# Kernel tuning notes

Measured on AMD Instinct MI355X. Metric: run time of the kernel, lower is better.

## Reference

```python
import jax, jax.numpy as jnp
import numpy as np

H = 512
B = 32
T = 2048


def setup_inputs() -> dict:
    key = jax.random.key(0)
    ks = jax.random.split(key, 8)
    hidden = jax.random.normal(ks[0], (1, B, H), dtype=jnp.float32)
    encoder_outputs = jax.random.normal(ks[1], (T, B, H), dtype=jnp.float32)
    coverage = jax.random.uniform(ks[2], (B, T), dtype=jnp.float32)
    # nn.Linear(3H, H): weight [H, 3H], bias [H]
    W_attn = jax.random.normal(ks[3], (H, 3 * H), dtype=jnp.float32) / np.sqrt(3 * H)
    b_attn = jax.random.normal(ks[4], (H,), dtype=jnp.float32) / np.sqrt(3 * H)
    # v ~ Normal(0, 1/sqrt(H))
    v = jax.random.normal(ks[5], (H,), dtype=jnp.float32) / np.sqrt(H)
    # nn.Linear(1, H, bias=False): weight [H, 1]
    W_cov = jax.random.normal(ks[6], (H, 1), dtype=jnp.float32)
    return {"hidden": hidden, "encoder_outputs": encoder_outputs, "coverage": coverage,
            "W_attn": W_attn, "b_attn": b_attn, "v": v, "W_cov": W_cov}


def reference(hidden, encoder_outputs, coverage, W_attn, b_attn, v, W_cov):
    # hidden: [1,B,H], encoder_outputs: [T,B,H], coverage: [B,T]
    enc = jnp.transpose(encoder_outputs, (1, 0, 2))          # [B,T,H]
    b, t, h = enc.shape
    hrep = jnp.broadcast_to(hidden[0][:, None, :], (b, t, h))  # [B,T,H]
    # coverage_feature = Linear(1,H,bias=False)(coverage[...,None]) -> outer product
    cov_feat = coverage[..., None] * W_cov[:, 0]               # [B,T,H]
    x = jnp.concatenate([hrep, enc, cov_feat], axis=-1)        # [B,T,3H]
    energy = jax.nn.relu(jnp.einsum('btk,hk->bth', x, W_attn) + b_attn)  # [B,T,H]
    scores = jnp.einsum('bth,h->bt', energy, v)                # [B,T]
    attn_weights = jax.nn.softmax(scores, axis=1)              # softmax over T
    coverage_new = coverage + attn_weights                     # [B,T]
    return attn_weights[:, None, :], coverage_new
```

## Files before the change

### kernel.cpp

```cpp
#include <hip/hip_runtime.h>
#include <hip/hip_bf16.h>

typedef unsigned short u16;
typedef __attribute__((ext_vector_type(8))) short bf16x8;
typedef __attribute__((ext_vector_type(4))) float f32x4;

#define T_DIM 2048
#define B_DIM 32
#define H_DIM 512
#define M_DIM (T_DIM * B_DIM)

__device__ inline unsigned pack2(float a, float b) {
  union { __hip_bfloat162 h2; unsigned u; } c;
  c.h2 = __float22bfloat162_rn(make_float2(a, b));
  return c.u;
}

__global__ __launch_bounds__(256) void prep_kernel(
    const float* __restrict__ hidden, const float* __restrict__ W_attn,
    const float* __restrict__ b_attn, const float* __restrict__ W_cov,
    u16* __restrict__ W2bf, float* __restrict__ r, float* __restrict__ u)
{
  const int tid = blockIdx.x * 256 + threadIdx.x;
  const int pair = tid >> 2;
  const int kq = tid & 3;
  const int b = pair >> 9, h = pair & 511;

  {
    const float* hid = hidden + b * 512 + kq * 128;
    const float* w1 = W_attn + (size_t)h * 1536 + kq * 128;
    float acc = 0.f;
    #pragma unroll 8
    for (int k = 0; k < 128; k += 4) {
      float4 x = *(const float4*)(hid + k);
      float4 w = *(const float4*)(w1 + k);
      acc += x.x * w.x + x.y * w.y + x.z * w.z + x.w * w.w;
    }
    acc += __shfl_xor(acc, 1);
    acc += __shfl_xor(acc, 2);
    if (kq == 0) r[pair] = acc + b_attn[h];
  }

  {
    int j0 = tid * 4;
    int hh = j0 >> 9, kk = j0 & 511;
    float4 w = *(const float4*)(W_attn + (size_t)hh * 1536 + 512 + kk);
    uint2 p;
    p.x = pack2(w.x, w.y);
    p.y = pack2(w.z, w.w);
    *(uint2*)&W2bf[j0] = p;
  }

  if (tid < 2048) {
    int h3 = tid >> 2;
    const float* w3 = W_attn + (size_t)h3 * 1536 + 1024 + kq * 128;
    const float* wc = W_cov + kq * 128;
    float su = 0.f;
    #pragma unroll 8
    for (int k = 0; k < 128; k += 4) {
      float4 a = *(const float4*)(w3 + k);
      float4 c = *(const float4*)(wc + k);
      su += a.x * c.x + a.y * c.y + a.z * c.z + a.w * c.w;
    }
    su += __shfl_xor(su, 1);
    su += __shfl_xor(su, 2);
    if (kq == 0) u[h3] = su;
  }
}

__global__ __launch_bounds__(256) void gemm_score(
    const float* __restrict__ enc, const u16* __restrict__ W2bf,
    const float* __restrict__ r, const float* __restrict__ u,
    const float* __restrict__ vv, const float* __restrict__ cov,
    float* __restrict__ part)
{
  const int n0 = blockIdx.x * 128;
  const int m0 = blockIdx.y * 128;
  const int tid = threadIdx.x;
  const int lane = tid & 63;
  const int wid = tid >> 6;
  const int wm = wid >> 1, wn = wid & 1;
  const int quad = lane >> 4, col = lane & 15;

  __shared__ u16 As[128 * 64];
  __shared__ u16 Bs[128 * 64];

  f32x4 acc[4][4] = {};

  for (int kb = 0; kb < 512; kb += 64) {
    #pragma unroll
    for (int it = 0; it < 4; ++it) {
      int un = tid + 256 * it;
      int row = un >> 3, ku = (un & 7) * 8;
      const float* ga = enc + (size_t)(m0 + row) * 512 + kb + ku;
      float4 f0 = *(const float4*)ga;
      float4 f1 = *(const float4*)(ga + 4);
      uint4 p;
      p.x = pack2(f0.x, f0.y);
      p.y = pack2(f0.z, f0.w);
      p.z = pack2(f1.x, f1.y);
      p.w = pack2(f1.z, f1.w);
      *(uint4*)&As[row * 64 + ku] = p;
    }
    #pragma unroll
    for (int it = 0; it < 4; ++it) {
      int c = tid + 256 * it;
      int row = c >> 3, kc = (c & 7) * 8;
      *(uint4*)&Bs[row * 64 + kc] =
          *(const uint4*)(W2bf + (size_t)(n0 + row) * 512 + kb + kc);
    }
    __syncthreads();
    #pragma unroll
    for (int ks = 0; ks < 64; ks += 32) {
      bf16x8 af[4], bfr[4];
      #pragma unroll
      for (int i = 0; i < 4; ++i)
        af[i] = *(const bf16x8*)&As[(wm * 64 + i * 16 + col) * 64 + ks + quad * 8];
      #pragma unroll
      for (int j = 0; j < 4; ++j)
        bfr[j] = *(const bf16x8*)&Bs[(wn * 64 + j * 16 + col) * 64 + ks + quad * 8];
      #pragma unroll
      for (int i = 0; i < 4; ++i)
        #pragma unroll
        for (int j = 0; j < 4; ++j)
          acc[i][j] = __builtin_amdgcn_mfma_f32_16x16x32_bf16(af[i], bfr[j], acc[i][j], 0, 0, 0);
    }
    __syncthreads();
  }

  float uj[4], vj[4];
  #pragma unroll
  for (int j = 0; j < 4; ++j) {
    int gh = n0 + wn * 64 + j * 16 + col;
    uj[j] = u[gh];
    vj[j] = vv[gh];
  }
  #pragma unroll
  for (int i = 0; i < 4; ++i) {
    float sarr[4];
    #pragma unroll
    for (int reg = 0; reg < 4; ++reg) {
      int gm = m0 + wm * 64 + i * 16 + quad * 4 + reg;
      int b = gm & 31, t = gm >> 5;
      float cv = cov[b * 2048 + t];
      const float* rb = r + b * 512;
      float sum = 0.f;
      #pragma unroll
      for (int j = 0; j < 4; ++j) {
        int gh = n0 + wn * 64 + j * 16 + col;
        float e = acc[i][j][reg] + rb[gh] + cv * uj[j];
        e = fmaxf(e, 0.f);
        sum += e * vj[j];
      }
      sum += __shfl_xor(sum, 1);
      sum += __shfl_xor(sum, 2);
      sum += __shfl_xor(sum, 4);
      sum += __shfl_xor(sum, 8);
      sarr[reg] = sum;
    }
    if (col < 4) {
      float val = (col == 0) ? sarr[0] : (col == 1) ? sarr[1] : (col == 2) ? sarr[2] : sarr[3];
      int gm = m0 + wm * 64 + i * 16 + quad * 4 + col;
      part[(size_t)(blockIdx.x * 2 + wn) * M_DIM + gm] = val;
    }
  }
}

__global__ __launch_bounds__(256) void softmax_kernel(
    const float* __restrict__ part, const float* __restrict__ cov, float* __restrict__ out)
{
  const int b = blockIdx.x;
  const int tid = threadIdx.x;
  const int lane = tid & 63, wid = tid >> 6;
  __shared__ float red[4];
  float loc[8];
  float lmax = -3.4e38f;
  #pragma unroll
  for (int i = 0; i < 8; ++i) {
    int t = tid + i * 256;
    float s = 0.f;
    #pragma unroll
    for (int p = 0; p < 8; ++p) s += part[(size_t)p * M_DIM + t * 32 + b];
    loc[i] = s;
    lmax = fmaxf(lmax, s);
  }
  #pragma unroll
  for (int o = 32; o; o >>= 1) lmax = fmaxf(lmax, __shfl_xor(lmax, o));
  if (lane == 0) red[wid] = lmax;
  __syncthreads();
  float bmax = fmaxf(fmaxf(red[0], red[1]), fmaxf(red[2], red[3]));
  __syncthreads();
  float lsum = 0.f;
  #pragma unroll
  for (int i = 0; i < 8; ++i) { loc[i] = __expf(loc[i] - bmax); lsum += loc[i]; }
  #pragma unroll
  for (int o = 32; o; o >>= 1) lsum += __shfl_xor(lsum, o);
  if (lane == 0) red[wid] = lsum;
  __syncthreads();
  float inv = 1.0f / (red[0] + red[1] + red[2] + red[3]);
  #pragma unroll
  for (int i = 0; i < 8; ++i) {
    int t = tid + i * 256;
    float a = loc[i] * inv;
    out[b * 2048 + t] = a;
    out[65536 + b * 2048 + t] = cov[b * 2048 + t] + a;
  }
}

extern "C" void kernel_launch(void* const* d_in, const int* in_sizes, int n_in,
                              void* d_out, int out_size, void* d_ws, size_t ws_size,
                              hipStream_t stream) {
  const float* hidden = (const float*)d_in[0];
  const float* enc    = (const float*)d_in[1];
  const float* cov    = (const float*)d_in[2];
  const float* W_attn = (const float*)d_in[3];
  const float* b_attn = (const float*)d_in[4];
  const float* vv     = (const float*)d_in[5];
  const float* W_cov  = (const float*)d_in[6];
  float* out = (float*)d_out;

  u16* W2bf = (u16*)d_ws;
  float* r  = (float*)((char*)d_ws + 512 * 1024);
  float* u  = r + 32 * 512;
  float* part = u + 512;

  hipLaunchKernelGGL(prep_kernel, dim3(256), dim3(256), 0, stream,
                     hidden, W_attn, b_attn, W_cov, W2bf, r, u);
  hipLaunchKernelGGL(gemm_score, dim3(4, 512), dim3(256), 0, stream,
                     enc, W2bf, r, u, vv, cov, part);
  hipLaunchKernelGGL(softmax_kernel, dim3(32), dim3(256), 0, stream,
                     part, cov, out);
}
```

Baseline: 292.5 us.

## Restructure score GEMM so each block covers full N with register-streamed weights

Each block now loads a 64-row slab of encoder outputs (full K=512) into XOR-swizzled LDS once. Each wave streams its 128-column slice of the bf16 weights straight from global/L2 into registers with one-step prefetching, instead of tiling over N across blocks. The original split re-read and re-converted the fp32 encoder rows four times across N-blocks, and this change removes that redundant traffic. The cost is 64 KB of LDS per block, higher register pressure from a 4x8 accumulator array, and every wave reading weights from L2. The partial-score layout is changed to [wave][b][t] and reduced over 4 partials in the softmax kernel.

```diff
diff --git a/kernel.cpp b/kernel.cpp
--- a/kernel.cpp
+++ b/kernel.cpp
@@ -68,100 +68,102 @@
   }
 }
 
-__global__ __launch_bounds__(256) void gemm_score(
+__global__ __launch_bounds__(256, 2) void gemm_score(
     const float* __restrict__ enc, const u16* __restrict__ W2bf,
     const float* __restrict__ r, const float* __restrict__ u,
     const float* __restrict__ vv, const float* __restrict__ cov,
     float* __restrict__ part)
 {
-  const int n0 = blockIdx.x * 128;
-  const int m0 = blockIdx.y * 128;
+  const int m0 = blockIdx.x * 64;
   const int tid = threadIdx.x;
   const int lane = tid & 63;
-  const int wid = tid >> 6;
-  const int wm = wid >> 1, wn = wid & 1;
+  const int w = tid >> 6;
   const int quad = lane >> 4, col = lane & 15;
 
-  __shared__ u16 As[128 * 64];
-  __shared__ u16 Bs[128 * 64];
-
-  f32x4 acc[4][4] = {};
-
-  for (int kb = 0; kb < 512; kb += 64) {
-    #pragma unroll
-    for (int it = 0; it < 4; ++it) {
-      int un = tid + 256 * it;
-      int row = un >> 3, ku = (un & 7) * 8;
-      const float* ga = enc + (size_t)(m0 + row) * 512 + kb + ku;
-      float4 f0 = *(const float4*)ga;
-      float4 f1 = *(const float4*)(ga + 4);
-      uint4 p;
-      p.x = pack2(f0.x, f0.y);
-      p.y = pack2(f0.z, f0.w);
-      p.z = pack2(f1.x, f1.y);
-      p.w = pack2(f1.z, f1.w);
-      *(uint4*)&As[row * 64 + ku] = p;
-    }
-    #pragma unroll
-    for (int it = 0; it < 4; ++it) {
-      int c = tid + 256 * it;
-      int row = c >> 3, kc = (c & 7) * 8;
-      *(uint4*)&Bs[row * 64 + kc] =
-          *(const uint4*)(W2bf + (size_t)(n0 + row) * 512 + kb + kc);
-    }
-    __syncthreads();
-    #pragma unroll
-    for (int ks = 0; ks < 64; ks += 32) {
-      bf16x8 af[4], bfr[4];
-      #pragma unroll
-      for (int i = 0; i < 4; ++i)
-        af[i] = *(const bf16x8*)&As[(wm * 64 + i * 16 + col) * 64 + ks + quad * 8];
-      #pragma unroll
-      for (int j = 0; j < 4; ++j)
-        bfr[j] = *(const bf16x8*)&Bs[(wn * 64 + j * 16 + col) * 64 + ks + quad * 8];
-      #pragma unroll
-      for (int i = 0; i < 4; ++i)
-        #pragma unroll
-        for (int j = 0; j < 4; ++j)
-          acc[i][j] = __builtin_amdgcn_mfma_f32_16x16x32_bf16(af[i], bfr[j], acc[i][j], 0, 0, 0);
-    }
-    __syncthreads();
-  }
-
-  float uj[4], vj[4];
-  #pragma unroll
-  for (int j = 0; j < 4; ++j) {
-    int gh = n0 + wn * 64 + j * 16 + col;
+  __shared__ u16 As[64 * 512];
+
+  #pragma unroll
+  for (int it = 0; it < 16; ++it) {
+    int un = tid + 256 * it;
+    int row = un >> 6;
+    int g = un & 63;
+    const float* ga = enc + (size_t)(m0 + row) * 512 + g * 8;
+    float4 f0 = *(const float4*)ga;
+    float4 f1 = *(const float4*)(ga + 4);
+    uint4 p;
+    p.x = pack2(f0.x, f0.y);
+    p.y = pack2(f0.z, f0.w);
+    p.z = pack2(f1.x, f1.y);
+    p.w = pack2(f1.z, f1.w);
+    *(uint4*)&As[row * 512 + (g ^ (row & 7)) * 8] = p;
+  }
+  __syncthreads();
+
+  f32x4 acc[4][8] = {};
+  const u16* bbase = W2bf + (size_t)(w * 128 + col) * 512 + quad * 8;
+
+  bf16x8 bcur[8], bnxt[8];
+  #pragma unroll
+  for (int j = 0; j < 8; ++j)
+    bcur[j] = *(const bf16x8*)(bbase + j * 16 * 512);
+
+  #pragma unroll
+  for (int ks = 0; ks < 16; ++ks) {
+    if (ks < 15) {
+      #pragma unroll
+      for (int j = 0; j < 8; ++j)
+        bnxt[j] = *(const bf16x8*)(bbase + j * 16 * 512 + (ks + 1) * 32);
+    }
+    bf16x8 af[4];
+    #pragma unroll
+    for (int i = 0; i < 4; ++i) {
+      int row = i * 16 + col;
+      af[i] = *(const bf16x8*)&As[row * 512 + (((ks * 4 + quad) ^ (col & 7))) * 8];
+    }
+    #pragma unroll
+    for (int i = 0; i < 4; ++i)
+      #pragma unroll
+      for (int j = 0; j < 8; ++j)
+        acc[i][j] = __builtin_amdgcn_mfma_f32_16x16x32_bf16(af[i], bcur[j], acc[i][j], 0, 0, 0);
+    #pragma unroll
+    for (int j = 0; j < 8; ++j) bcur[j] = bnxt[j];
+  }
+
+  float uj[8], vj[8];
+  #pragma unroll
+  for (int j = 0; j < 8; ++j) {
+    int gh = w * 128 + j * 16 + col;
     uj[j] = u[gh];
     vj[j] = vv[gh];
   }
   #pragma unroll
-  for (int i = 0; i < 4; ++i) {
-    float sarr[4];
+  for (int ih = 0; ih < 2; ++ih) {
     #pragma unroll
     for (int reg = 0; reg < 4; ++reg) {
-      int gm = m0 + wm * 64 + i * 16 + quad * 4 + reg;
-      int b = gm & 31, t = gm >> 5;
-      float cv = cov[b * 2048 + t];
+      int b = (ih * 16 + quad * 4 + reg) & 31;
       const float* rb = r + b * 512;
-      float sum = 0.f;
-      #pragma unroll
-      for (int j = 0; j < 4; ++j) {
-        int gh = n0 + wn * 64 + j * 16 + col;
-        float e = acc[i][j][reg] + rb[gh] + cv * uj[j];
-        e = fmaxf(e, 0.f);
-        sum += e * vj[j];
+      float rbj[8];
+      #pragma unroll
+      for (int j = 0; j < 8; ++j) rbj[j] = rb[w * 128 + j * 16 + col];
+      #pragma unroll
+      for (int isub = 0; isub < 2; ++isub) {
+        int i = ih + isub * 2;
+        int m = m0 + i * 16 + quad * 4 + reg;
+        int t = m >> 5;
+        float cv = cov[b * 2048 + t];
+        float s = 0.f;
+        #pragma unroll
+        for (int j = 0; j < 8; ++j) {
+          float e = acc[i][j][reg] + rbj[j] + cv * uj[j];
+          e = fmaxf(e, 0.f);
+          s += e * vj[j];
+        }
+        s += __shfl_xor(s, 1);
+        s += __shfl_xor(s, 2);
+        s += __shfl_xor(s, 4);
+        s += __shfl_xor(s, 8);
+        if (col == 0) part[(size_t)(w * 32 + b) * 2048 + t] = s;
       }
-      sum += __shfl_xor(sum, 1);
-      sum += __shfl_xor(sum, 2);
-      sum += __shfl_xor(sum, 4);
-      sum += __shfl_xor(sum, 8);
-      sarr[reg] = sum;
-    }
-    if (col < 4) {
-      float val = (col == 0) ? sarr[0] : (col == 1) ? sarr[1] : (col == 2) ? sarr[2] : sarr[3];
-      int gm = m0 + wm * 64 + i * 16 + quad * 4 + col;
-      part[(size_t)(blockIdx.x * 2 + wn) * M_DIM + gm] = val;
     }
   }
 }
@@ -180,7 +182,7 @@
     int t = tid + i * 256;
     float s = 0.f;
     #pragma unroll
-    for (int p = 0; p < 8; ++p) s += part[(size_t)p * M_DIM + t * 32 + b];
+    for (int p = 0; p < 4; ++p) s += part[(size_t)(p * 32 + b) * 2048 + t];
     loc[i] = s;
     lmax = fmaxf(lmax, s);
   }
@@ -226,7 +228,7 @@
 
   hipLaunchKernelGGL(prep_kernel, dim3(256), dim3(256), 0, stream,
                      hidden, W_attn, b_attn, W_cov, W2bf, r, u);
-  hipLaunchKernelGGL(gemm_score, dim3(4, 512), dim3(256), 0, stream,
+  hipLaunchKernelGGL(gemm_score, dim3(1024), dim3(256), 0, stream,
                      enc, W2bf, r, u, vv, cov, part);
   hipLaunchKernelGGL(softmax_kernel, dim3(32), dim3(256), 0, stream,
                      part, cov, out);
```

Result: faster. 281.7 us (-3.7%).
